# Optimization experiments

Hardware: AMD Instinct MI355X
Metric: run time of the kernel (lower is better)

The kernel has to match this reference:

```python
import jax, jax.numpy as jnp
import numpy as np

EMBED_DIM = 512


def setup_inputs() -> dict:
    key = jax.random.key(0)
    k1, k2, k3 = jax.random.split(key, 3)
    B, T, E = 8, 2048, EMBED_DIM
    x = jax.random.normal(k1, (B, T, E), dtype=jnp.float32)
    # Linear weights stored [in, out] (torch stores [out, in]; math is identical via transpose)
    Wq = jax.random.normal(k2, (E, E), dtype=jnp.float32) * (E ** -0.5)
    bq = jnp.zeros((E,), dtype=jnp.float32)
    Wk = jax.random.normal(k3, (E, E), dtype=jnp.float32) * (E ** -0.5)
    bk = jnp.zeros((E,), dtype=jnp.float32)
    return {"x": x, "Wq": Wq, "bq": bq, "Wk": Wk, "bk": bk}


def reference(x, Wq, bq, Wk, bk) -> jnp.ndarray:
    scaling = jnp.float32(EMBED_DIM ** -0.5)
    q = (x @ Wq + bq) * scaling          # [B, T, E]
    k = x @ Wk + bk                       # [B, T, E]
    scores = jnp.einsum("bqe,bke->bqk", q, k)   # [B, T, T]
    attn = jax.nn.softmax(scores, axis=-1)
    return jnp.einsum("bqk,bke->bqe", attn, x)  # V = x
```

## Files before the change

### kernel.cpp

```cpp
#include <hip/hip_runtime.h>
#include <hip/hip_bf16.h>
#include <stdint.h>

#define B_  8
#define T_  2048
#define E_  512

typedef __attribute__((ext_vector_type(8))) __bf16 bf16x8;
typedef __attribute__((ext_vector_type(8))) unsigned short ushort8;
typedef __attribute__((ext_vector_type(4))) unsigned short ushort4v;
typedef __attribute__((ext_vector_type(4))) float f32x4;

__device__ __forceinline__ float bf2f(unsigned short u) {
  union { unsigned int u; float f; } c; c.u = ((unsigned int)u) << 16; return c.f;
}
__device__ __forceinline__ unsigned short f2bf(float f) {
  union { float f; unsigned int u; } c; c.f = f;
  unsigned int u = c.u;
  unsigned int r = (u + 0x7FFFu + ((u >> 16) & 1u)) >> 16;
  return (unsigned short)r;
}

__device__ __forceinline__ void gload_lds16(const void* g, void* l) {
  __builtin_amdgcn_global_load_lds(
      (const __attribute__((address_space(1))) uint32_t*)g,
      (__attribute__((address_space(3))) uint32_t*)l, 16, 0, 0);
}

__global__ __launch_bounds__(256)
void trans_conv_kernel(const float* __restrict__ x, unsigned short* __restrict__ xbf,
                       unsigned short* __restrict__ xT) {
  __shared__ unsigned short tile[64][66];
  const int t0 = blockIdx.x * 64, e0 = blockIdx.y * 64, b = blockIdx.z;
  const int tid = threadIdx.x;
  const float* xb = x + ((size_t)b * T_ + t0) * E_ + e0;
  unsigned short* xbf_b = xbf + ((size_t)b * T_ + t0) * E_ + e0;
#pragma unroll
  for (int it = 0; it < 4; ++it) {
    int tr = (tid >> 4) + it * 16;
    int ec = (tid & 15) * 4;
    float4 f = *reinterpret_cast<const float4*>(xb + (size_t)tr * E_ + ec);
    ushort4v o;
    o[0] = f2bf(f.x); o[1] = f2bf(f.y); o[2] = f2bf(f.z); o[3] = f2bf(f.w);
    *reinterpret_cast<ushort4v*>(xbf_b + (size_t)tr * E_ + ec) = o;
    tile[ec + 0][tr] = o[0];
    tile[ec + 1][tr] = o[1];
    tile[ec + 2][tr] = o[2];
    tile[ec + 3][tr] = o[3];
  }
  __syncthreads();
  unsigned short* dst = xT + ((size_t)b * E_ + e0) * T_ + t0;
#pragma unroll
  for (int it = 0; it < 2; ++it) {
    int er = (tid >> 3) + it * 32;
    int tg = (tid & 7) * 8;
    ushort8 r;
#pragma unroll
    for (int j = 0; j < 8; ++j) r[j] = tile[er][tg + j];
    *reinterpret_cast<ushort8*>(dst + (size_t)er * T_ + tg) = r;
  }
}

__global__ __launch_bounds__(256)
void conv_w_kernel(const float* __restrict__ Wq, const float* __restrict__ Wk,
                   const float* __restrict__ bq, const float* __restrict__ bk,
                   unsigned short* __restrict__ WT, float* __restrict__ bqk, float scale) {
  int idx = blockIdx.x * 256 + threadIdx.x;
  int n  = idx >> 9;
  int kk = idx & 511;
  float v = (n < E_) ? Wq[kk * E_ + n] * scale : Wk[kk * E_ + (n - E_)];
  WT[idx] = f2bf(v);
  if (idx < 2 * E_) {
    float bv = (idx < E_) ? bq[idx] * scale : bk[idx - E_];
    bqk[idx] = bv;
  }
}

#define READ_A(pp, ha) do {                                                    \
  const int rbase = (pp) * 32768 + aRow + (ha) * 4096;                         \
  _Pragma("unroll") for (int m = 0; m < 4; ++m) {                              \
    aA[m][0] = *reinterpret_cast<const bf16x8*>(&sm[rbase + m * 1024 + aCol0]);\
    aA[m][1] = *reinterpret_cast<const bf16x8*>(&sm[rbase + m * 1024 + aCol1]);\
  } } while (0)

#define READ_B(pp, hb) do {                                                    \
  const int rbase = (pp) * 32768 + bRow + (hb) * 2048;                         \
  _Pragma("unroll") for (int n = 0; n < 2; ++n) {                              \
    bB[hb][n][0] = *reinterpret_cast<const bf16x8*>(&sm[rbase + n * 1024 + aCol0]);\
    bB[hb][n][1] = *reinterpret_cast<const bf16x8*>(&sm[rbase + n * 1024 + aCol1]);\
  } } while (0)

#define MFMA_Q(ha, hb) do {                                                    \
  _Pragma("unroll") for (int m = 0; m < 4; ++m)                                \
  _Pragma("unroll") for (int n = 0; n < 2; ++n) {                              \
    acc[(ha)*4+m][(hb)*2+n] = __builtin_amdgcn_mfma_f32_16x16x32_bf16(         \
        aA[m][0], bB[hb][n][0], acc[(ha)*4+m][(hb)*2+n], 0, 0, 0);             \
    acc[(ha)*4+m][(hb)*2+n] = __builtin_amdgcn_mfma_f32_16x16x32_bf16(         \
        aA[m][1], bB[hb][n][1], acc[(ha)*4+m][(hb)*2+n], 0, 0, 0);             \
  } } while (0)

#define STAGE_OP(gptr, ld, base, kt) do {                                      \
  _Pragma("unroll") for (int h = 0; h < 2; ++h)                                \
  _Pragma("unroll") for (int rr2 = 0; rr2 < 2; ++rr2)                          \
    gload_lds16(gptr + (long long)(h * 128 + rr2 * 64) * (ld) + (long long)(kt) * 64, \
                &sm[(base) + h * 8192 + rr2 * 4096 + wv * 512]);               \
  } while (0)

template<int OUT_BF16, int DO_EXP>
__global__ __launch_bounds__(512)
void gemm256(const unsigned short* __restrict__ A, int lda, long long strA,
             const unsigned short* __restrict__ B, int ldb, long long strB,
             void* __restrict__ Cv, int ldc, long long strC,
             int K, const float* __restrict__ bias, int NBX, int NBY,
             float* __restrict__ Rg)
{
  __shared__ unsigned short sm[65536];
  const int tid  = threadIdx.x;
  const int lane = tid & 63;
  const int wv   = tid >> 6;
  const int wr   = wv >> 2;
  const int wc   = wv & 3;
  const int fr   = lane & 15;

  const int nwg = gridDim.x, bid = blockIdx.x;
  const int qq = nwg >> 3, rr = nwg & 7, xc = bid & 7, ii = bid >> 3;
  const int wg = (xc < rr ? xc * (qq + 1) : rr * (qq + 1) + (xc - rr) * qq) + ii;
  const int bx = wg % NBX;
  const int tt = wg / NBX;
  const int by = tt % NBY;
  const int bz = tt / NBY;

  const long long m0 = (long long)by * 256;
  const long long n0 = (long long)bx * 256;
  const unsigned short* Ab = A + (long long)bz * strA + m0 * lda;
  const unsigned short* Bb = B + (long long)bz * strB + n0 * ldb;

  const int srow = tid >> 3;
  const int scol = ((tid & 7) * 8) ^ ((srow & 7) << 3);
  const unsigned short* gA = Ab + (long long)srow * lda + scol;
  const unsigned short* gB = Bb + (long long)srow * ldb + scol;

  const int xorc  = (fr & 7) << 3;
  const int q8    = (lane >> 4) * 8;
  const int aCol0 = (q8) ^ xorc;
  const int aCol1 = (32 + q8) ^ xorc;
  const int aRow  = (wr * 128 + fr) * 64;
  const int bRow  = 16384 + (wc * 64 + fr) * 64;

  f32x4 acc[8][4];
#pragma unroll
  for (int i = 0; i < 8; ++i)
#pragma unroll
    for (int j = 0; j < 4; ++j) acc[i][j] = (f32x4){0.f, 0.f, 0.f, 0.f};

  bf16x8 aA[4][2], bB[2][2][2];
  const int NT = K >> 6;

  STAGE_OP(gA, lda, 0, 0);
  STAGE_OP(gB, ldb, 16384, 0);
  asm volatile("s_waitcnt vmcnt(0)" ::: "memory");
  __builtin_amdgcn_s_barrier();

  int p = 0;
  for (int kt = 0; kt < NT; ++kt) {
    const int pn = p ^ 1;
    const int pnb = pn * 32768;
    READ_A(p, 0);
    READ_B(p, 0);
    if (kt + 1 < NT) STAGE_OP(gA, lda, pnb, kt + 1);
    __builtin_amdgcn_s_barrier();
    __builtin_amdgcn_s_setprio(1); MFMA_Q(0, 0); __builtin_amdgcn_s_setprio(0);
    __builtin_amdgcn_s_barrier();
    READ_B(p, 1);
    if (kt + 1 < NT) STAGE_OP(gB, ldb, pnb + 16384, kt + 1);
    __builtin_amdgcn_s_barrier();
    __builtin_amdgcn_s_setprio(1); MFMA_Q(0, 1); __builtin_amdgcn_s_setprio(0);
    __builtin_amdgcn_s_barrier();
    READ_A(p, 1);
    __builtin_amdgcn_s_barrier();
    __builtin_amdgcn_s_setprio(1); MFMA_Q(1, 0); __builtin_amdgcn_s_setprio(0);
    __builtin_amdgcn_s_barrier();
    __builtin_amdgcn_s_setprio(1); MFMA_Q(1, 1); __builtin_amdgcn_s_setprio(0);
    asm volatile("s_waitcnt vmcnt(0)" ::: "memory");
    __builtin_amdgcn_s_barrier();
    p = pn;
  }

  const int rq = (lane >> 4) * 4;
  if (bias) {
#pragma unroll
    for (int nn = 0; nn < 4; ++nn) {
      const float bv = bias[n0 + wc * 64 + (nn >> 1) * 32 + (nn & 1) * 16 + fr];
#pragma unroll
      for (int mm = 0; mm < 8; ++mm)
#pragma unroll
        for (int j = 0; j < 4; ++j) acc[mm][nn][j] += bv;
    }
  }
  if (DO_EXP) {
#pragma unroll
    for (int mm = 0; mm < 8; ++mm)
#pragma unroll
      for (int nn = 0; nn < 4; ++nn)
#pragma unroll
        for (int j = 0; j < 4; ++j) acc[mm][nn][j] = __expf(acc[mm][nn][j]);
  }
  if (OUT_BF16) {
    unsigned short* C = (unsigned short*)Cv + (long long)bz * strC;
#pragma unroll
    for (int mm = 0; mm < 8; ++mm)
#pragma unroll
      for (int j = 0; j < 4; ++j) {
        const long long row = m0 + wr * 128 + (mm >> 2) * 64 + (mm & 3) * 16 + rq + j;
#pragma unroll
        for (int nn = 0; nn < 4; ++nn) {
          const long long col = n0 + wc * 64 + (nn >> 1) * 32 + (nn & 1) * 16 + fr;
          C[row * ldc + col] = f2bf(acc[mm][nn][j]);
        }
      }
  } else {
    float* C = (float*)Cv + (long long)bz * strC;
#pragma unroll
    for (int mm = 0; mm < 8; ++mm)
#pragma unroll
      for (int j = 0; j < 4; ++j) {
        const long long row = m0 + wr * 128 + (mm >> 2) * 64 + (mm & 3) * 16 + rq + j;
#pragma unroll
        for (int nn = 0; nn < 4; ++nn) {
          const long long col = n0 + wc * 64 + (nn >> 1) * 32 + (nn & 1) * 16 + fr;
          C[row * ldc + col] = acc[mm][nn][j];
        }
      }
  }
  if (DO_EXP) {
    float* rps = (float*)sm;
    __syncthreads();
#pragma unroll
    for (int mm = 0; mm < 8; ++mm)
#pragma unroll
      for (int j = 0; j < 4; ++j) {
        float s = acc[mm][0][j] + acc[mm][1][j] + acc[mm][2][j] + acc[mm][3][j];
        s += __shfl_xor(s, 1); s += __shfl_xor(s, 2);
        s += __shfl_xor(s, 4); s += __shfl_xor(s, 8);
        const int lrow = wr * 128 + (mm >> 2) * 64 + (mm & 3) * 16 + rq + j;
        if (fr == 0) rps[wc * 256 + lrow] = s;
      }
    __syncthreads();
    if (tid < 256) {
      const float s = rps[tid] + rps[256 + tid] + rps[512 + tid] + rps[768 + tid];
      Rg[((long long)bz * NBX + bx) * 2048 + m0 + tid] = s;
    }
  }
}

__global__ __launch_bounds__(256)
void rowsum_inv_kernel(const float* __restrict__ R, float* __restrict__ invR) {
  const int i = blockIdx.x * 256 + threadIdx.x;
  const int b = i >> 11, t = i & 2047;
  float s = 0.f;
#pragma unroll
  for (int c = 0; c < 8; ++c) s += R[((long long)(b * 8 + c)) * 2048 + t];
  invR[i] = 1.0f / s;
}

__global__ __launch_bounds__(256)
void gemm_pv2(const unsigned short* __restrict__ A, int lda, long long strA,
              const unsigned short* __restrict__ B, int ldb, long long strB,
              const float* __restrict__ invR,
              float* __restrict__ C, int ldc, long long strC, int K)
{
  __shared__ unsigned short sm[32768];
  const int tid  = threadIdx.x;
  const int lane = tid & 63;
  const int wv   = tid >> 6;
  const int wrp  = wv >> 1;
  const int wcp  = wv & 1;
  const int fr   = lane & 15;

  const int nwg = gridDim.x, bid = blockIdx.x;
  const int qq = nwg >> 3, rr = nwg & 7, xc = bid & 7, ii = bid >> 3;
  const int wg = (xc < rr ? xc * (qq + 1) : rr * (qq + 1) + (xc - rr) * qq) + ii;
  const int bx = wg & 3;
  const int by = (wg >> 2) & 15;
  const int bz = wg >> 6;

  const long long m0 = (long long)by * 128;
  const long long n0 = (long long)bx * 128;
  const unsigned short* Ab = A + (long long)bz * strA + m0 * lda;
  const unsigned short* Bb = B + (long long)bz * strB + n0 * ldb;

  const int srow = tid >> 3;
  const int scol = ((tid & 7) * 8) ^ ((srow & 7) << 3);
  const unsigned short* gA = Ab + (long long)srow * lda + scol;
  const unsigned short* gB = Bb + (long long)srow * ldb + scol;

  const int xorc  = (fr & 7) << 3;
  const int q8    = (lane >> 4) * 8;
  const int c0    = q8 ^ xorc;
  const int c1    = (32 + q8) ^ xorc;
  const int aRow  = (wrp * 64 + fr) * 64;
  const int bRow  = 8192 + (wcp * 64 + fr) * 64;

  f32x4 acc[4][4];
#pragma unroll
  for (int i = 0; i < 4; ++i)
#pragma unroll
    for (int j = 0; j < 4; ++j) acc[i][j] = (f32x4){0.f, 0.f, 0.f, 0.f};

  bf16x8 aA[4][2], bB2[2][2];
  const int NT = K >> 6;

#pragma unroll
  for (int r = 0; r < 4; ++r)
    gload_lds16(gA + (long long)(r * 32) * lda, &sm[r * 2048 + tid * 8]);
#pragma unroll
  for (int r = 0; r < 4; ++r)
    gload_lds16(gB + (long long)(r * 32) * ldb, &sm[8192 + r * 2048 + tid * 8]);
  asm volatile("s_waitcnt vmcnt(0)" ::: "memory");
  __builtin_amdgcn_s_barrier();

  int p = 0;
  for (int kt = 0; kt < NT; ++kt) {
    const int pb = p * 16384, pnb = pb ^ 16384;
    const long long koff = (long long)(kt + 1) * 64;
#pragma unroll
    for (int m = 0; m < 4; ++m) {
      aA[m][0] = *reinterpret_cast<const bf16x8*>(&sm[pb + aRow + m * 1024 + c0]);
      aA[m][1] = *reinterpret_cast<const bf16x8*>(&sm[pb + aRow + m * 1024 + c1]);
    }
#pragma unroll
    for (int n = 0; n < 2; ++n) {
      bB2[n][0] = *reinterpret_cast<const bf16x8*>(&sm[pb + bRow + n * 1024 + c0]);
      bB2[n][1] = *reinterpret_cast<const bf16x8*>(&sm[pb + bRow + n * 1024 + c1]);
    }
    if (kt + 1 < NT) {
#pragma unroll
      for (int r = 0; r < 4; ++r)
        gload_lds16(gA + (long long)(r * 32) * lda + koff, &sm[pnb + r * 2048 + tid * 8]);
    }
    __builtin_amdgcn_s_barrier();
    __builtin_amdgcn_s_setprio(1);
#pragma unroll
    for (int m = 0; m < 4; ++m)
#pragma unroll
      for (int n = 0; n < 2; ++n) {
        acc[m][n] = __builtin_amdgcn_mfma_f32_16x16x32_bf16(aA[m][0], bB2[n][0], acc[m][n], 0, 0, 0);
        acc[m][n] = __builtin_amdgcn_mfma_f32_16x16x32_bf16(aA[m][1], bB2[n][1], acc[m][n], 0, 0, 0);
      }
    __builtin_amdgcn_s_setprio(0);
    __builtin_amdgcn_s_barrier();
#pragma unroll
    for (int n = 0; n < 2; ++n) {
      bB2[n][0] = *reinterpret_cast<const bf16x8*>(&sm[pb + bRow + (2 + n) * 1024 + c0]);
      bB2[n][1] = *reinterpret_cast<const bf16x8*>(&sm[pb + bRow + (2 + n) * 1024 + c1]);
    }
    if (kt + 1 < NT) {
#pragma unroll
      for (int r = 0; r < 4; ++r)
        gload_lds16(gB + (long long)(r * 32) * ldb + koff, &sm[pnb + 8192 + r * 2048 + tid * 8]);
    }
    __builtin_amdgcn_s_barrier();
    __builtin_amdgcn_s_setprio(1);
#pragma unroll
    for (int m = 0; m < 4; ++m)
#pragma unroll
      for (int n = 0; n < 2; ++n) {
        acc[m][2 + n] = __builtin_amdgcn_mfma_f32_16x16x32_bf16(aA[m][0], bB2[n][0], acc[m][2 + n], 0, 0, 0);
        acc[m][2 + n] = __builtin_amdgcn_mfma_f32_16x16x32_bf16(aA[m][1], bB2[n][1], acc[m][2 + n], 0, 0, 0);
      }
    __builtin_amdgcn_s_setprio(0);
    asm volatile("s_waitcnt vmcnt(0)" ::: "memory");
    __builtin_amdgcn_s_barrier();
    p ^= 1;
  }

  const int rq = (lane >> 4) * 4;
  float* Cb = C + (long long)bz * strC;
#pragma unroll
  for (int m = 0; m < 4; ++m)
#pragma unroll
    for (int j = 0; j < 4; ++j) {
      const int lrow = wrp * 64 + m * 16 + rq + j;
      const long long row = m0 + lrow;
      const float inv = invR[bz * 2048 + row];
#pragma unroll
      for (int n = 0; n < 4; ++n)
        Cb[row * ldc + n0 + wcp * 64 + n * 16 + fr] = acc[m][n][j] * inv;
    }
}

extern "C" void kernel_launch(void* const* d_in, const int* in_sizes, int n_in,
                              void* d_out, int out_size, void* d_ws, size_t ws_size,
                              hipStream_t stream)
{
  const float* x  = (const float*)d_in[0];
  const float* Wq = (const float*)d_in[1];
  const float* bq = (const float*)d_in[2];
  const float* Wk = (const float*)d_in[3];
  const float* bk = (const float*)d_in[4];
  float* out = (float*)d_out;

  char* w = (char*)d_ws;
  unsigned short* xbf  = (unsigned short*)w;  w += (size_t)B_ * T_ * E_ * 2;
  unsigned short* xT   = (unsigned short*)w;  w += (size_t)B_ * T_ * E_ * 2;
  unsigned short* WT   = (unsigned short*)w;  w += (size_t)2 * E_ * E_ * 2;
  float*          bqk  = (float*)w;           w += (size_t)2 * E_ * 4;
  float*          R    = (float*)w;           w += (size_t)B_ * 8 * T_ * 4;
  float*          invR = (float*)w;           w += (size_t)B_ * T_ * 4;
  unsigned short* qk   = (unsigned short*)w;  w += (size_t)B_ * T_ * 2 * E_ * 2;
  unsigned short* attn = (unsigned short*)w;  w += (size_t)B_ * T_ * T_ * 2;

  const float scale = 0.044194173824159216f;

  trans_conv_kernel<<<dim3(32, 8, 8), 256, 0, stream>>>(x, xbf, xT);
  conv_w_kernel<<<2048, 256, 0, stream>>>(Wq, Wk, bq, bk, WT, bqk, scale);

  gemm256<1, 0><<<256, 512, 0, stream>>>(
      xbf, E_, 0, WT, E_, 0, qk, 2 * E_, 0, E_, bqk, 4, 64, nullptr);

  gemm256<1, 1><<<512, 512, 0, stream>>>(
      qk, 2 * E_, (long long)T_ * 2 * E_,
      qk + E_, 2 * E_, (long long)T_ * 2 * E_,
      attn, T_, (long long)T_ * T_, E_, nullptr, 8, 8, R);

  rowsum_inv_kernel<<<64, 256, 0, stream>>>(R, invR);

  gemm_pv2<<<512, 256, 0, stream>>>(
      attn, T_, (long long)T_ * T_,
      xT, T_, (long long)E_ * T_,
      invR, out, E_, (long long)T_ * E_, T_);
}
```

Before: 139.5 us.

## Shrink QK and projection GEMM tiles to 128x128 with LDS-staged coalesced stores

Replaces the 256x256, 512-thread GEMM with a 128x128, 256-thread variant for both the Q/K projection and the score/exp GEMM, quadrupling the grid and halving LDS use so more workgroups can be resident per CU. The epilogue now stages bf16 results through padded LDS and writes 16-byte coalesced rows instead of scattered 2-byte stores. Row-sum partials double to 16 per row, and the rowsum kernel and workspace are updated to match. Smaller tiles lower operand reuse and raise global and L2 traffic per FLOP.

```diff
diff --git a/kernel.cpp b/kernel.cpp
--- a/kernel.cpp
+++ b/kernel.cpp
@@ -76,50 +76,20 @@
   }
 }
 
-#define READ_A(pp, ha) do {                                                    \
-  const int rbase = (pp) * 32768 + aRow + (ha) * 4096;                         \
-  _Pragma("unroll") for (int m = 0; m < 4; ++m) {                              \
-    aA[m][0] = *reinterpret_cast<const bf16x8*>(&sm[rbase + m * 1024 + aCol0]);\
-    aA[m][1] = *reinterpret_cast<const bf16x8*>(&sm[rbase + m * 1024 + aCol1]);\
-  } } while (0)
-
-#define READ_B(pp, hb) do {                                                    \
-  const int rbase = (pp) * 32768 + bRow + (hb) * 2048;                         \
-  _Pragma("unroll") for (int n = 0; n < 2; ++n) {                              \
-    bB[hb][n][0] = *reinterpret_cast<const bf16x8*>(&sm[rbase + n * 1024 + aCol0]);\
-    bB[hb][n][1] = *reinterpret_cast<const bf16x8*>(&sm[rbase + n * 1024 + aCol1]);\
-  } } while (0)
-
-#define MFMA_Q(ha, hb) do {                                                    \
-  _Pragma("unroll") for (int m = 0; m < 4; ++m)                                \
-  _Pragma("unroll") for (int n = 0; n < 2; ++n) {                              \
-    acc[(ha)*4+m][(hb)*2+n] = __builtin_amdgcn_mfma_f32_16x16x32_bf16(         \
-        aA[m][0], bB[hb][n][0], acc[(ha)*4+m][(hb)*2+n], 0, 0, 0);             \
-    acc[(ha)*4+m][(hb)*2+n] = __builtin_amdgcn_mfma_f32_16x16x32_bf16(         \
-        aA[m][1], bB[hb][n][1], acc[(ha)*4+m][(hb)*2+n], 0, 0, 0);             \
-  } } while (0)
-
-#define STAGE_OP(gptr, ld, base, kt) do {                                      \
-  _Pragma("unroll") for (int h = 0; h < 2; ++h)                                \
-  _Pragma("unroll") for (int rr2 = 0; rr2 < 2; ++rr2)                          \
-    gload_lds16(gptr + (long long)(h * 128 + rr2 * 64) * (ld) + (long long)(kt) * 64, \
-                &sm[(base) + h * 8192 + rr2 * 4096 + wv * 512]);               \
-  } while (0)
-
-template<int OUT_BF16, int DO_EXP>
-__global__ __launch_bounds__(512)
-void gemm256(const unsigned short* __restrict__ A, int lda, long long strA,
+template<int DO_EXP>
+__global__ __launch_bounds__(256)
+void gemm128(const unsigned short* __restrict__ A, int lda, long long strA,
              const unsigned short* __restrict__ B, int ldb, long long strB,
-             void* __restrict__ Cv, int ldc, long long strC,
+             unsigned short* __restrict__ Cg, int ldc, long long strC,
              int K, const float* __restrict__ bias, int NBX, int NBY,
              float* __restrict__ Rg)
 {
-  __shared__ unsigned short sm[65536];
+  __shared__ unsigned short sm[32768];
   const int tid  = threadIdx.x;
   const int lane = tid & 63;
   const int wv   = tid >> 6;
-  const int wr   = wv >> 2;
-  const int wc   = wv & 3;
+  const int wrp  = wv >> 1;
+  const int wcp  = wv & 1;
   const int fr   = lane & 15;
 
   const int nwg = gridDim.x, bid = blockIdx.x;
@@ -130,8 +100,8 @@
   const int by = tt % NBY;
   const int bz = tt / NBY;
 
-  const long long m0 = (long long)by * 256;
-  const long long n0 = (long long)bx * 256;
+  const long long m0 = (long long)by * 128;
+  const long long n0 = (long long)bx * 128;
   const unsigned short* Ab = A + (long long)bz * strA + m0 * lda;
   const unsigned short* Bb = B + (long long)bz * strB + n0 * ldb;
 
@@ -142,114 +112,136 @@
 
   const int xorc  = (fr & 7) << 3;
   const int q8    = (lane >> 4) * 8;
-  const int aCol0 = (q8) ^ xorc;
-  const int aCol1 = (32 + q8) ^ xorc;
-  const int aRow  = (wr * 128 + fr) * 64;
-  const int bRow  = 16384 + (wc * 64 + fr) * 64;
-
-  f32x4 acc[8][4];
-#pragma unroll
-  for (int i = 0; i < 8; ++i)
+  const int c0    = q8 ^ xorc;
+  const int c1    = (32 + q8) ^ xorc;
+  const int aRow  = (wrp * 64 + fr) * 64;
+  const int bRow  = 8192 + (wcp * 64 + fr) * 64;
+
+  f32x4 acc[4][4];
+#pragma unroll
+  for (int i = 0; i < 4; ++i)
 #pragma unroll
     for (int j = 0; j < 4; ++j) acc[i][j] = (f32x4){0.f, 0.f, 0.f, 0.f};
 
-  bf16x8 aA[4][2], bB[2][2][2];
+  bf16x8 aA[4][2], bB2[2][2];
   const int NT = K >> 6;
 
-  STAGE_OP(gA, lda, 0, 0);
-  STAGE_OP(gB, ldb, 16384, 0);
+#pragma unroll
+  for (int r = 0; r < 4; ++r)
+    gload_lds16(gA + (long long)(r * 32) * lda, &sm[r * 2048 + tid * 8]);
+#pragma unroll
+  for (int r = 0; r < 4; ++r)
+    gload_lds16(gB + (long long)(r * 32) * ldb, &sm[8192 + r * 2048 + tid * 8]);
   asm volatile("s_waitcnt vmcnt(0)" ::: "memory");
   __builtin_amdgcn_s_barrier();
 
   int p = 0;
   for (int kt = 0; kt < NT; ++kt) {
-    const int pn = p ^ 1;
-    const int pnb = pn * 32768;
-    READ_A(p, 0);
-    READ_B(p, 0);
-    if (kt + 1 < NT) STAGE_OP(gA, lda, pnb, kt + 1);
-    __builtin_amdgcn_s_barrier();
-    __builtin_amdgcn_s_setprio(1); MFMA_Q(0, 0); __builtin_amdgcn_s_setprio(0);
-    __builtin_amdgcn_s_barrier();
-    READ_B(p, 1);
-    if (kt + 1 < NT) STAGE_OP(gB, ldb, pnb + 16384, kt + 1);
-    __builtin_amdgcn_s_barrier();
-    __builtin_amdgcn_s_setprio(1); MFMA_Q(0, 1); __builtin_amdgcn_s_setprio(0);
-    __builtin_amdgcn_s_barrier();
-    READ_A(p, 1);
-    __builtin_amdgcn_s_barrier();
-    __builtin_amdgcn_s_setprio(1); MFMA_Q(1, 0); __builtin_amdgcn_s_setprio(0);
-    __builtin_amdgcn_s_barrier();
-    __builtin_amdgcn_s_setprio(1); MFMA_Q(1, 1); __builtin_amdgcn_s_setprio(0);
+    const int pb = p * 16384, pnb = pb ^ 16384;
+    const long long koff = (long long)(kt + 1) * 64;
+#pragma unroll
+    for (int m = 0; m < 4; ++m) {
+      aA[m][0] = *reinterpret_cast<const bf16x8*>(&sm[pb + aRow + m * 1024 + c0]);
+      aA[m][1] = *reinterpret_cast<const bf16x8*>(&sm[pb + aRow + m * 1024 + c1]);
+    }
+#pragma unroll
+    for (int n = 0; n < 2; ++n) {
+      bB2[n][0] = *reinterpret_cast<const bf16x8*>(&sm[pb + bRow + n * 1024 + c0]);
+      bB2[n][1] = *reinterpret_cast<const bf16x8*>(&sm[pb + bRow + n * 1024 + c1]);
+    }
+    if (kt + 1 < NT) {
+#pragma unroll
+      for (int r = 0; r < 4; ++r)
+        gload_lds16(gA + (long long)(r * 32) * lda + koff, &sm[pnb + r * 2048 + tid * 8]);
+    }
+    __builtin_amdgcn_s_barrier();
+    __builtin_amdgcn_s_setprio(1);
+#pragma unroll
+    for (int m = 0; m < 4; ++m)
+#pragma unroll
+      for (int n = 0; n < 2; ++n) {
+        acc[m][n] = __builtin_amdgcn_mfma_f32_16x16x32_bf16(aA[m][0], bB2[n][0], acc[m][n], 0, 0, 0);
+        acc[m][n] = __builtin_amdgcn_mfma_f32_16x16x32_bf16(aA[m][1], bB2[n][1], acc[m][n], 0, 0, 0);
+      }
+    __builtin_amdgcn_s_setprio(0);
+    __builtin_amdgcn_s_barrier();
+#pragma unroll
+    for (int n = 0; n < 2; ++n) {
+      bB2[n][0] = *reinterpret_cast<const bf16x8*>(&sm[pb + bRow + (2 + n) * 1024 + c0]);
+      bB2[n][1] = *reinterpret_cast<const bf16x8*>(&sm[pb + bRow + (2 + n) * 1024 + c1]);
+    }
+    if (kt + 1 < NT) {
+#pragma unroll
+      for (int r = 0; r < 4; ++r)
+        gload_lds16(gB + (long long)(r * 32) * ldb + koff, &sm[pnb + 8192 + r * 2048 + tid * 8]);
+    }
+    __builtin_amdgcn_s_barrier();
+    __builtin_amdgcn_s_setprio(1);
+#pragma unroll
+    for (int m = 0; m < 4; ++m)
+#pragma unroll
+      for (int n = 0; n < 2; ++n) {
+        acc[m][2 + n] = __builtin_amdgcn_mfma_f32_16x16x32_bf16(aA[m][0], bB2[n][0], acc[m][2 + n], 0, 0, 0);
+        acc[m][2 + n] = __builtin_amdgcn_mfma_f32_16x16x32_bf16(aA[m][1], bB2[n][1], acc[m][2 + n], 0, 0, 0);
+      }
+    __builtin_amdgcn_s_setprio(0);
     asm volatile("s_waitcnt vmcnt(0)" ::: "memory");
     __builtin_amdgcn_s_barrier();
-    p = pn;
+    p ^= 1;
   }
 
   const int rq = (lane >> 4) * 4;
-  if (bias) {
-#pragma unroll
-    for (int nn = 0; nn < 4; ++nn) {
-      const float bv = bias[n0 + wc * 64 + (nn >> 1) * 32 + (nn & 1) * 16 + fr];
-#pragma unroll
-      for (int mm = 0; mm < 8; ++mm)
-#pragma unroll
-        for (int j = 0; j < 4; ++j) acc[mm][nn][j] += bv;
-    }
-  }
   if (DO_EXP) {
 #pragma unroll
-    for (int mm = 0; mm < 8; ++mm)
-#pragma unroll
-      for (int nn = 0; nn < 4; ++nn)
-#pragma unroll
-        for (int j = 0; j < 4; ++j) acc[mm][nn][j] = __expf(acc[mm][nn][j]);
-  }
-  if (OUT_BF16) {
-    unsigned short* C = (unsigned short*)Cv + (long long)bz * strC;
-#pragma unroll
-    for (int mm = 0; mm < 8; ++mm)
+    for (int m = 0; m < 4; ++m)
+#pragma unroll
+      for (int n = 0; n < 4; ++n)
+#pragma unroll
+        for (int j = 0; j < 4; ++j) acc[m][n][j] = __expf(acc[m][n][j]);
+    float* rps = (float*)(sm + 17664);
+#pragma unroll
+    for (int m = 0; m < 4; ++m)
 #pragma unroll
       for (int j = 0; j < 4; ++j) {
-        const long long row = m0 + wr * 128 + (mm >> 2) * 64 + (mm & 3) * 16 + rq + j;
-#pragma unroll
-        for (int nn = 0; nn < 4; ++nn) {
-          const long long col = n0 + wc * 64 + (nn >> 1) * 32 + (nn & 1) * 16 + fr;
-          C[row * ldc + col] = f2bf(acc[mm][nn][j]);
-        }
-      }
-  } else {
-    float* C = (float*)Cv + (long long)bz * strC;
-#pragma unroll
-    for (int mm = 0; mm < 8; ++mm)
-#pragma unroll
-      for (int j = 0; j < 4; ++j) {
-        const long long row = m0 + wr * 128 + (mm >> 2) * 64 + (mm & 3) * 16 + rq + j;
-#pragma unroll
-        for (int nn = 0; nn < 4; ++nn) {
-          const long long col = n0 + wc * 64 + (nn >> 1) * 32 + (nn & 1) * 16 + fr;
-          C[row * ldc + col] = acc[mm][nn][j];
-        }
-      }
-  }
-  if (DO_EXP) {
-    float* rps = (float*)sm;
-    __syncthreads();
-#pragma unroll
-    for (int mm = 0; mm < 8; ++mm)
-#pragma unroll
-      for (int j = 0; j < 4; ++j) {
-        float s = acc[mm][0][j] + acc[mm][1][j] + acc[mm][2][j] + acc[mm][3][j];
+        float s = acc[m][0][j] + acc[m][1][j] + acc[m][2][j] + acc[m][3][j];
         s += __shfl_xor(s, 1); s += __shfl_xor(s, 2);
         s += __shfl_xor(s, 4); s += __shfl_xor(s, 8);
-        const int lrow = wr * 128 + (mm >> 2) * 64 + (mm & 3) * 16 + rq + j;
-        if (fr == 0) rps[wc * 256 + lrow] = s;
+        if (fr == 0) rps[wcp * 128 + wrp * 64 + m * 16 + rq + j] = s;
       }
-    __syncthreads();
-    if (tid < 256) {
-      const float s = rps[tid] + rps[256 + tid] + rps[512 + tid] + rps[768 + tid];
+  } else if (bias) {
+#pragma unroll
+    for (int n = 0; n < 4; ++n) {
+      const float bv = bias[n0 + wcp * 64 + n * 16 + fr];
+#pragma unroll
+      for (int m = 0; m < 4; ++m)
+#pragma unroll
+        for (int j = 0; j < 4; ++j) acc[m][n][j] += bv;
+    }
+  }
+#pragma unroll
+  for (int m = 0; m < 4; ++m)
+#pragma unroll
+    for (int j = 0; j < 4; ++j) {
+      const int lrow = wrp * 64 + m * 16 + rq + j;
+#pragma unroll
+      for (int n = 0; n < 4; ++n)
+        sm[lrow * 136 + wcp * 64 + n * 16 + fr] = f2bf(acc[m][n][j]);
+    }
+  __syncthreads();
+  if (DO_EXP) {
+    float* rps = (float*)(sm + 17664);
+    if (tid < 128) {
+      const float s = rps[tid] + rps[128 + tid];
       Rg[((long long)bz * NBX + bx) * 2048 + m0 + tid] = s;
     }
+  }
+  unsigned short* C = Cg + (long long)bz * strC;
+#pragma unroll
+  for (int it = 0; it < 8; ++it) {
+    const int row = it * 16 + (tid >> 4);
+    const int chunk = tid & 15;
+    ushort8 v = *reinterpret_cast<const ushort8*>(&sm[row * 136 + chunk * 8]);
+    *reinterpret_cast<ushort8*>(&C[(m0 + row) * ldc + n0 + chunk * 8]) = v;
   }
 }
 
@@ -259,7 +251,7 @@
   const int b = i >> 11, t = i & 2047;
   float s = 0.f;
 #pragma unroll
-  for (int c = 0; c < 8; ++c) s += R[((long long)(b * 8 + c)) * 2048 + t];
+  for (int c = 0; c < 16; ++c) s += R[((long long)(b * 16 + c)) * 2048 + t];
   invR[i] = 1.0f / s;
 }
 
@@ -405,7 +397,7 @@
   unsigned short* xT   = (unsigned short*)w;  w += (size_t)B_ * T_ * E_ * 2;
   unsigned short* WT   = (unsigned short*)w;  w += (size_t)2 * E_ * E_ * 2;
   float*          bqk  = (float*)w;           w += (size_t)2 * E_ * 4;
-  float*          R    = (float*)w;           w += (size_t)B_ * 8 * T_ * 4;
+  float*          R    = (float*)w;           w += (size_t)B_ * 16 * T_ * 4;
   float*          invR = (float*)w;           w += (size_t)B_ * T_ * 4;
   unsigned short* qk   = (unsigned short*)w;  w += (size_t)B_ * T_ * 2 * E_ * 2;
   unsigned short* attn = (unsigned short*)w;  w += (size_t)B_ * T_ * T_ * 2;
@@ -415,13 +407,13 @@
   trans_conv_kernel<<<dim3(32, 8, 8), 256, 0, stream>>>(x, xbf, xT);
   conv_w_kernel<<<2048, 256, 0, stream>>>(Wq, Wk, bq, bk, WT, bqk, scale);
 
-  gemm256<1, 0><<<256, 512, 0, stream>>>(
-      xbf, E_, 0, WT, E_, 0, qk, 2 * E_, 0, E_, bqk, 4, 64, nullptr);
-
-  gemm256<1, 1><<<512, 512, 0, stream>>>(
+  gemm128<0><<<1024, 256, 0, stream>>>(
+      xbf, E_, 0, WT, E_, 0, qk, 2 * E_, 0, E_, bqk, 8, 128, nullptr);
+
+  gemm128<1><<<2048, 256, 0, stream>>>(
       qk, 2 * E_, (long long)T_ * 2 * E_,
       qk + E_, 2 * E_, (long long)T_ * 2 * E_,
-      attn, T_, (long long)T_ * T_, E_, nullptr, 8, 8, R);
+      attn, T_, (long long)T_ * T_, E_, nullptr, 16, 16, R);
 
   rowsum_inv_kernel<<<64, 256, 0, stream>>>(R, invR);
 
```

Result: no change. 139.5 us (+0.0%).
